# Kernel tuning notes

Hardware: AMD Instinct MI355X
Metric: run time of the kernel (lower is better)

Reference implementation:

```python
import jax, jax.numpy as jnp
import numpy as np

D_MODEL = 512
NUM_HEADS = 8
D_K = D_MODEL // NUM_HEADS


def setup_inputs() -> dict:
    key = jax.random.key(0)
    k0, k1, k2, k3, k4 = jax.random.split(key, 5)
    s = 1.0 / np.sqrt(D_MODEL)
    return {
        "x": jax.random.normal(k0, (2, 4096, D_MODEL), dtype=jnp.float32),
        "W_q": jax.random.normal(k1, (D_MODEL, D_MODEL), dtype=jnp.float32) * s,
        "W_k": jax.random.normal(k2, (D_MODEL, D_MODEL), dtype=jnp.float32) * s,
        "W_v": jax.random.normal(k3, (D_MODEL, D_MODEL), dtype=jnp.float32) * s,
        "W_o": jax.random.normal(k4, (D_MODEL, D_MODEL), dtype=jnp.float32) * s,
    }


def reference(x, W_q, W_k, W_v, W_o):
    B, S, _ = x.shape
    # project and split heads: (B, H, S, d_k)
    def split(t):
        return t.reshape(B, S, NUM_HEADS, D_K).transpose(0, 2, 1, 3)
    Q = split(x @ W_q)
    K = split(x @ W_k)
    V = split(x @ W_v)
    scale = jnp.sqrt(jnp.asarray(D_K, dtype=x.dtype))
    logits = jnp.einsum('bhqd,bhkd->bhqk', Q, K) / scale
    attn = jax.nn.softmax(logits, axis=-1)  # dropout is identity at inference
    out = jnp.einsum('bhqk,bhkd->bhqd', attn, V)
    concat = out.transpose(0, 2, 1, 3).reshape(B, S, D_MODEL)
    return concat @ W_o
```

## Files before the change

kernel.cpp:

```cpp
#include <hip/hip_runtime.h>
#include <hip/hip_bf16.h>


#define DMODEL 512
#define SEQ    4096
#define NTOK   8192
#define LDQK   1024

using f32x4 = __attribute__((ext_vector_type(4))) float;
using s16x8 = __attribute__((ext_vector_type(8))) short;
using u16x8 = __attribute__((ext_vector_type(8))) unsigned short;

static __device__ __forceinline__ unsigned short f2bf(float f) {
  union { float f; unsigned u; } v; v.f = f;
  unsigned r = v.u + 0x7fff + ((v.u >> 16) & 1);
  return (unsigned short)(r >> 16);
}

static __device__ __forceinline__ unsigned pack_bf2(float lo, float hi) {
  __hip_bfloat162 t = __float22bfloat162_rn(make_float2(lo, hi));
  union { __hip_bfloat162 b; unsigned u; } c; c.b = t; return c.u;
}

static __device__ __forceinline__ void gll16(const void* g, void* l) {
  __builtin_amdgcn_global_load_lds(
      (const __attribute__((address_space(1))) unsigned int*)g,
      (__attribute__((address_space(3))) unsigned int*)l, 16, 0, 0);
}

__global__ void prep_kernel(const float* __restrict__ x,
                            const float* __restrict__ Wq,
                            const float* __restrict__ Wk,
                            const float* __restrict__ Wv,
                            const float* __restrict__ Wo,
                            unsigned short* __restrict__ xb,
                            unsigned short* __restrict__ Wall, float c2) {
  __shared__ float T[64][65];
  const int bx = blockIdx.x;
  if (bx < 1024) {
    for (int i = bx * 256 + threadIdx.x; i < NTOK * DMODEL / 4; i += 262144) {
      float4 v = ((const float4*)x)[i];
      ushort4 o;
      o.x = f2bf(v.x); o.y = f2bf(v.y); o.z = f2bf(v.z); o.w = f2bf(v.w);
      ((ushort4*)xb)[i] = o;
    }
    return;
  }
  const int t = bx - 1024;
  const int y = t >> 6, sub = t & 63;
  const float* W = (y == 0) ? Wq : (y == 1) ? Wk : (y == 2) ? Wv : Wo;
  const float scale = (y == 0) ? c2 : 1.0f;
  const int tk = (sub & 7) * 64;
  const int tn = (sub >> 3) * 64;
  const int r  = threadIdx.x >> 2;
  const int cq = threadIdx.x & 3;
#pragma unroll
  for (int i = 0; i < 4; ++i) {
    int c = (cq + 4 * i) * 4;
    float4 v = *(const float4*)&W[(size_t)(tk + r) * 512 + tn + c];
    T[r][c + 0] = v.x * scale; T[r][c + 1] = v.y * scale;
    T[r][c + 2] = v.z * scale; T[r][c + 3] = v.w * scale;
  }
  __syncthreads();
  const int n  = threadIdx.x >> 2;
  const int k0 = (threadIdx.x & 3) * 16;
#pragma unroll
  for (int j4 = 0; j4 < 4; ++j4) {
    ushort4 o;
    o.x = f2bf(T[k0 + j4 * 4 + 0][n]);
    o.y = f2bf(T[k0 + j4 * 4 + 1][n]);
    o.z = f2bf(T[k0 + j4 * 4 + 2][n]);
    o.w = f2bf(T[k0 + j4 * 4 + 3][n]);
    *(ushort4*)&Wall[(size_t)y * 262144 + (size_t)(tn + n) * 512 + tk + k0 + j4 * 4] = o;
  }
}

__global__ __launch_bounds__(256, 3) void gemm_qkv(
    const unsigned short* __restrict__ xb,
    const unsigned short* __restrict__ Wall,
    unsigned short* __restrict__ QKb,
    unsigned short* __restrict__ Vtb)
{
  __shared__ unsigned short As[128 * 32];
  __shared__ unsigned short Bs[128 * 32];
  const int by = blockIdx.y;
  const bool vmode = (by >= 8);
  const unsigned short* A  = vmode ? (Wall + 2 * 262144) : xb;
  const unsigned short* Bt = vmode ? xb : Wall;
  const size_t bm = vmode ? (size_t)(by - 8) * 128 : (size_t)blockIdx.x * 128;
  const size_t bn = vmode ? (size_t)blockIdx.x * 128 : (size_t)by * 128;
  const int tid  = threadIdx.x;
  const int wave = tid >> 6, lane = tid & 63;
  const int q4 = lane >> 4, ln = lane & 15;
  const int wm = (wave >> 1) * 64, wn = (wave & 1) * 64;
  f32x4 acc[4][4] = {};
  const int srow = wave * 16 + (lane >> 2);
  const int scol = (lane & 3) * 8;

  const unsigned short* Ag  = A  + (bm + srow)      * 512 + scol;
  const unsigned short* Ag2 = A  + (bm + 64 + srow) * 512 + scol;
  const unsigned short* Bg  = Bt + (bn + srow)      * 512 + scol;
  const unsigned short* Bg2 = Bt + (bn + 64 + srow) * 512 + scol;
  unsigned short* Ad  = As + wave * 512;
  unsigned short* Ad2 = As + 2048 + wave * 512;
  unsigned short* Bd  = Bs + wave * 512;
  unsigned short* Bd2 = Bs + 2048 + wave * 512;

  for (int kt = 0; kt < 512; kt += 32) {
    __syncthreads();
    gll16(Ag + kt,  Ad);
    gll16(Ag2 + kt, Ad2);
    gll16(Bg + kt,  Bd);
    gll16(Bg2 + kt, Bd2);
    __syncthreads();
    s16x8 af[4], bfr[4];
#pragma unroll
    for (int i = 0; i < 4; i++)
      af[i] = *(const s16x8*)(As + (wm + i * 16 + ln) * 32 + q4 * 8);
#pragma unroll
    for (int i = 0; i < 4; i++)
      bfr[i] = *(const s16x8*)(Bs + (wn + i * 16 + ln) * 32 + q4 * 8);
#pragma unroll
    for (int mi = 0; mi < 4; mi++)
#pragma unroll
      for (int ni = 0; ni < 4; ni++)
        acc[mi][ni] = __builtin_amdgcn_mfma_f32_16x16x32_bf16(
            af[mi], bfr[ni], acc[mi][ni], 0, 0, 0);
  }
#pragma unroll
  for (int mi = 0; mi < 4; mi++)
#pragma unroll
    for (int r = 0; r < 4; ++r) {
      size_t row = bm + wm + mi * 16 + q4 * 4 + r;
#pragma unroll
      for (int ni = 0; ni < 4; ni++) {
        size_t col = bn + wn + ni * 16 + ln;
        unsigned short hv = f2bf(acc[mi][ni][r]);
        if (!vmode) {
          QKb[row * 1024 + col] = hv;
        } else {
          int b = (int)(col >> 12), s = (int)(col & 4095);
          int sp = (s & ~63) | (s & 32) | (((s >> 2) & 3) << 3) |
                   (((s >> 4) & 1) << 2) | (s & 3);
          Vtb[(size_t)b * 2097152 + row * 4096 + sp] = hv;
        }
      }
    }
}

__global__ __launch_bounds__(256, 2) void attn_kernel(
    const unsigned short* __restrict__ QK,
    const unsigned short* __restrict__ Vt,
    float* __restrict__ Opart,
    float* __restrict__ Lpart)
{
  const int qt = blockIdx.x, h = blockIdx.y, z = blockIdx.z;
  const int b = z >> 1, ck = z & 1;
  const int tid = threadIdx.x, wave = tid >> 6, lane = tid & 63;
  const int q4 = lane >> 4, ln = lane & 15;
  __shared__ unsigned short Ks[2][64 * 64];
  __shared__ unsigned short Vs[2][64 * 64];
  const size_t rowbase = (size_t)b * SEQ;
  const size_t qrow0   = (size_t)qt * 128 + wave * 32;
  const unsigned short* Kp  = QK + rowbase * LDQK + 512 + h * 64;
  const unsigned short* VTp = Vt + ((size_t)(b * 8 + h) * 64) * SEQ;

  s16x8 qf[2][2];
#pragma unroll
  for (int mf = 0; mf < 2; ++mf) {
    const unsigned short* q = QK + (rowbase + qrow0 + mf * 16 + ln) * LDQK + h * 64;
    qf[mf][0] = *(const s16x8*)(q + q4 * 8);
    qf[mf][1] = *(const s16x8*)(q + 32 + q4 * 8);
  }
  f32x4 o[2][4] = {};
  float lp[2] = {};

  const int srow = tid >> 2;
  const int c32  = (tid & 3) * 32;
  const int swz  = (srow & 7) << 4;
  const int wof0 = srow * 128 + ((c32 +  0) ^ swz);
  const int wof1 = srow * 128 + ((c32 + 16) ^ swz);
  const int rswz = (ln & 7) << 4;

  const unsigned short* kgp = Kp  + (size_t)(ck * 2048 + srow) * LDQK + (c32 >> 1);
  const unsigned short* vgp = VTp + (size_t)srow * SEQ + ck * 2048 + (c32 >> 1);

  u16x8 kr  = *(const u16x8*)kgp;
  u16x8 kr2 = *(const u16x8*)(kgp + 8);
  u16x8 vr  = *(const u16x8*)vgp;
  u16x8 vr2 = *(const u16x8*)(vgp + 8);
  *(u16x8*)((char*)Ks[0] + wof0) = kr;
  *(u16x8*)((char*)Ks[0] + wof1) = kr2;
  *(u16x8*)((char*)Vs[0] + wof0) = vr;
  *(u16x8*)((char*)Vs[0] + wof1) = vr2;
  kgp += (size_t)64 * LDQK;  vgp += 64;
  kr  = *(const u16x8*)kgp;
  kr2 = *(const u16x8*)(kgp + 8);
  vr  = *(const u16x8*)vgp;
  vr2 = *(const u16x8*)(vgp + 8);
  __syncthreads();

  const f32x4 fz = {0.f, 0.f, 0.f, 0.f};

  for (int t = 0; t < 32; ++t) {
    const int cur = t & 1;
    const char* Kc = (const char*)Ks[cur];
    const char* Vc = (const char*)Vs[cur];

    f32x4 s4[2][4];
#pragma unroll
    for (int ni = 0; ni < 4; ni++) {
      const char* kb = Kc + (ni * 16 + ln) * 128;
      s16x8 kf0 = *(const s16x8*)(kb + ((q4 * 16)      ^ rswz));
      s16x8 kf1 = *(const s16x8*)(kb + ((q4 * 16 + 64) ^ rswz));
      __builtin_amdgcn_s_setprio(1);
#pragma unroll
      for (int mf = 0; mf < 2; ++mf) {
        f32x4 acc0 = __builtin_amdgcn_mfma_f32_16x16x32_bf16(kf0, qf[mf][0], fz, 0, 0, 0);
        s4[mf][ni] = __builtin_amdgcn_mfma_f32_16x16x32_bf16(kf1, qf[mf][1], acc0, 0, 0, 0);
      }
      __builtin_amdgcn_s_setprio(0);
    }
    s16x8 vf[2][4];
#pragma unroll
    for (int ks = 0; ks < 2; ++ks)
#pragma unroll
      for (int ni = 0; ni < 4; ni++)
        vf[ks][ni] = *(const s16x8*)(Vc + (ni * 16 + ln) * 128 +
                                     ((ks * 64 + q4 * 16) ^ rswz));

    s16x8 pf[2][2];
#pragma unroll
    for (int mf = 0; mf < 2; ++mf) {
      float e[4][4];
#pragma unroll
      for (int ni = 0; ni < 4; ni++)
#pragma unroll
        for (int r = 0; r < 4; ++r)
          e[ni][r] = __builtin_amdgcn_exp2f(s4[mf][ni][r]);
      float t0 = (e[0][0] + e[0][1]) + (e[0][2] + e[0][3]);
      float t1 = (e[1][0] + e[1][1]) + (e[1][2] + e[1][3]);
      float t2 = (e[2][0] + e[2][1]) + (e[2][2] + e[2][3]);
      float t3 = (e[3][0] + e[3][1]) + (e[3][2] + e[3][3]);
      lp[mf] += (t0 + t1) + (t2 + t3);
#pragma unroll
      for (int ks = 0; ks < 2; ++ks) {
        union { s16x8 v; unsigned u[4]; } pu;
        pu.u[0] = pack_bf2(e[2 * ks][0],     e[2 * ks][1]);
        pu.u[1] = pack_bf2(e[2 * ks][2],     e[2 * ks][3]);
        pu.u[2] = pack_bf2(e[2 * ks + 1][0], e[2 * ks + 1][1]);
        pu.u[3] = pack_bf2(e[2 * ks + 1][2], e[2 * ks + 1][3]);
        pf[mf][ks] = pu.v;
      }
    }
    __builtin_amdgcn_s_setprio(1);
#pragma unroll
    for (int ks = 0; ks < 2; ++ks)
#pragma unroll
      for (int ni = 0; ni < 4; ni++)
#pragma unroll
        for (int mf = 0; mf < 2; ++mf)
          o[mf][ni] = __builtin_amdgcn_mfma_f32_16x16x32_bf16(pf[mf][ks], vf[ks][ni], o[mf][ni], 0, 0, 0);
    __builtin_amdgcn_s_setprio(0);

    if (t + 1 < 32) {
      char* Kn = (char*)Ks[cur ^ 1];
      char* Vn = (char*)Vs[cur ^ 1];
      *(u16x8*)(Kn + wof0) = kr;
      *(u16x8*)(Kn + wof1) = kr2;
      *(u16x8*)(Vn + wof0) = vr;
      *(u16x8*)(Vn + wof1) = vr2;
      if (t + 2 < 32) {
        kgp += (size_t)64 * LDQK;  vgp += 64;
        kr  = *(const u16x8*)kgp;
        kr2 = *(const u16x8*)(kgp + 8);
        vr  = *(const u16x8*)vgp;
        vr2 = *(const u16x8*)(vgp + 8);
      }
    }
    __syncthreads();
  }
#pragma unroll
  for (int mf = 0; mf < 2; ++mf) {
    float l = lp[mf];
    l += __shfl_xor(l, 16, 64);
    l += __shfl_xor(l, 32, 64);
    if (q4 == 0)
      Lpart[(size_t)ck * 65536 + (size_t)(b * 8 + h) * 4096 + qrow0 + mf * 16 + ln] = l;
  }
  float* Opc = Opart + (size_t)ck * NTOK * DMODEL;
#pragma unroll
  for (int mf = 0; mf < 2; ++mf)
#pragma unroll
    for (int r = 0; r < 4; ++r) {
      size_t row = rowbase + qrow0 + mf * 16 + q4 * 4 + r;
#pragma unroll
      for (int ni = 0; ni < 4; ni++)
        Opc[row * DMODEL + h * 64 + ni * 16 + ln] = o[mf][ni][r];
    }
}

__global__ void combine_kernel(const float* __restrict__ Opart,
                               const float* __restrict__ Lpart,
                               unsigned short* __restrict__ Oc) {
  int i = blockIdx.x * 256 + threadIdx.x;
  int row = i >> 7;
  int c4  = (i & 127) * 4;
  int b = row >> 12, qrow = row & 4095, h = c4 >> 6;
  float l = Lpart[(size_t)(b * 8 + h) * 4096 + qrow] +
            Lpart[65536 + (size_t)(b * 8 + h) * 4096 + qrow];
  float inv = 1.0f / l;
  f32x4 a = *(const f32x4*)(Opart + (size_t)row * 512 + c4);
  f32x4 c = *(const f32x4*)(Opart + (size_t)NTOK * DMODEL + (size_t)row * 512 + c4);
  float r0 = (a[0] + c[0]) * inv, r1 = (a[1] + c[1]) * inv;
  float r2 = (a[2] + c[2]) * inv, r3 = (a[3] + c[3]) * inv;
  uint2 w;
  w.x = pack_bf2(r0, r1);
  w.y = pack_bf2(r2, r3);
  *(uint2*)&Oc[(size_t)row * 512 + c4] = w;
}

__global__ __launch_bounds__(256, 3) void gemm_out(
    const unsigned short* __restrict__ A,
    const unsigned short* __restrict__ Bt,
    float* __restrict__ C)
{
  __shared__ unsigned short As[128 * 32];
  __shared__ unsigned short Bs[64 * 32];
  const int tid  = threadIdx.x;
  const int wave = tid >> 6, lane = tid & 63;
  const int q4 = lane >> 4, ln = lane & 15;
  const size_t bm = (size_t)blockIdx.x * 128;
  const size_t bn = (size_t)blockIdx.y * 64;
  const int wm = (wave >> 1) * 64, wn = (wave & 1) * 32;
  f32x4 acc[4][2] = {};
  const int srow = wave * 16 + (lane >> 2);
  const int scol = (lane & 3) * 8;

  const unsigned short* Ag  = A  + (bm + srow)      * 512 + scol;
  const unsigned short* Ag2 = A  + (bm + 64 + srow) * 512 + scol;
  const unsigned short* Bg  = Bt + (bn + srow)      * 512 + scol;
  unsigned short* Ad  = As + wave * 512;
  unsigned short* Ad2 = As + 2048 + wave * 512;
  unsigned short* Bd  = Bs + wave * 512;

  for (int kt = 0; kt < 512; kt += 32) {
    __syncthreads();
    gll16(Ag + kt,  Ad);
    gll16(Ag2 + kt, Ad2);
    gll16(Bg + kt,  Bd);
    __syncthreads();
    s16x8 af[4], bfr[2];
#pragma unroll
    for (int i = 0; i < 4; i++)
      af[i] = *(const s16x8*)(As + (wm + i * 16 + ln) * 32 + q4 * 8);
#pragma unroll
    for (int i = 0; i < 2; i++)
      bfr[i] = *(const s16x8*)(Bs + (wn + i * 16 + ln) * 32 + q4 * 8);
#pragma unroll
    for (int mi = 0; mi < 4; mi++)
#pragma unroll
      for (int ni = 0; ni < 2; ni++)
        acc[mi][ni] = __builtin_amdgcn_mfma_f32_16x16x32_bf16(
            af[mi], bfr[ni], acc[mi][ni], 0, 0, 0);
  }
#pragma unroll
  for (int mi = 0; mi < 4; mi++)
#pragma unroll
    for (int r = 0; r < 4; ++r) {
      size_t row = bm + wm + mi * 16 + q4 * 4 + r;
#pragma unroll
      for (int ni = 0; ni < 2; ni++)
        C[row * 512 + bn + wn + ni * 16 + ln] = acc[mi][ni][r];
    }
}

extern "C" void kernel_launch(void* const* d_in, const int* in_sizes, int n_in,
                              void* d_out, int out_size, void* d_ws, size_t ws_size,
                              hipStream_t stream) {
  const float* x  = (const float*)d_in[0];
  const float* Wq = (const float*)d_in[1];
  const float* Wk = (const float*)d_in[2];
  const float* Wv = (const float*)d_in[3];
  const float* Wo = (const float*)d_in[4];

  char* ws = (char*)d_ws;
  unsigned short* xb    = (unsigned short*)(ws);
  unsigned short* Wall  = (unsigned short*)(ws + 8388608);
  unsigned short* QKb   = (unsigned short*)(ws + 10485760);
  unsigned short* Vtb   = (unsigned short*)(ws + 27262976);
  unsigned short* Oc    = (unsigned short*)(ws + 35651584);
  float*          Opart = (float*)(ws + 44040192);
  float*          Lpart = (float*)(ws + 77594624);

  const float C2 = 0.125f * 1.44269504088896f;

  hipLaunchKernelGGL(prep_kernel, dim3(1280), dim3(256), 0, stream,
                     x, Wq, Wk, Wv, Wo, xb, Wall, C2);
  hipLaunchKernelGGL(gemm_qkv, dim3(64, 12), dim3(256), 0, stream,
                     xb, Wall, QKb, Vtb);
  hipLaunchKernelGGL(attn_kernel, dim3(32, 8, 4), dim3(256), 0, stream,
                     QKb, Vtb, Opart, Lpart);
  hipLaunchKernelGGL(combine_kernel, dim3(4096), dim3(256), 0, stream,
                     Opart, Lpart, Oc);
  hipLaunchKernelGGL(gemm_out, dim3(64, 8), dim3(256), 0, stream,
                     Oc, Wall + 3 * 262144, (float*)d_out);
}
```

Before: 193.2 us.

## Drop split-K attention and fuse normalization into attention epilogue

The attention kernel no longer splits the key range in two. Each block now handles 64 query rows (16 per wave) across all 4096 keys and writes normalized bf16 output directly, so the combine kernel and the fp32 partial O/L buffers are removed. The grid is remapped with a block-index swizzle so blocks sharing a head run close together, and launch bounds are raised to 4 blocks per CU. This removes a launch and the fp32 partial write/read traffic. In exchange, K/V tiles are reused across fewer query rows, so K/V loads per unit of work double, and each block runs twice as many loop iterations.

Result: slower. 203.3 us (+5.2%).

```diff
diff --git a/kernel.cpp b/kernel.cpp
--- a/kernel.cpp
+++ b/kernel.cpp
@@ -148,32 +148,31 @@
     }
 }
 
-__global__ __launch_bounds__(256, 2) void attn_kernel(
+__global__ __launch_bounds__(256, 4) void attn_kernel(
     const unsigned short* __restrict__ QK,
     const unsigned short* __restrict__ Vt,
-    float* __restrict__ Opart,
-    float* __restrict__ Lpart)
+    unsigned short* __restrict__ Oc)
 {
-  const int qt = blockIdx.x, h = blockIdx.y, z = blockIdx.z;
-  const int b = z >> 1, ck = z & 1;
+  const int bid = blockIdx.x + 64 * (blockIdx.y + 8 * blockIdx.z);
+  const int lin = (bid & 7) * 128 + (bid >> 3);
+  const int qt = lin & 63, h = (lin >> 6) & 7, b = lin >> 9;
   const int tid = threadIdx.x, wave = tid >> 6, lane = tid & 63;
   const int q4 = lane >> 4, ln = lane & 15;
   __shared__ unsigned short Ks[2][64 * 64];
   __shared__ unsigned short Vs[2][64 * 64];
   const size_t rowbase = (size_t)b * SEQ;
-  const size_t qrow0   = (size_t)qt * 128 + wave * 32;
+  const size_t qrow0   = (size_t)qt * 64 + wave * 16;
   const unsigned short* Kp  = QK + rowbase * LDQK + 512 + h * 64;
   const unsigned short* VTp = Vt + ((size_t)(b * 8 + h) * 64) * SEQ;
 
-  s16x8 qf[2][2];
-#pragma unroll
-  for (int mf = 0; mf < 2; ++mf) {
-    const unsigned short* q = QK + (rowbase + qrow0 + mf * 16 + ln) * LDQK + h * 64;
-    qf[mf][0] = *(const s16x8*)(q + q4 * 8);
-    qf[mf][1] = *(const s16x8*)(q + 32 + q4 * 8);
-  }
-  f32x4 o[2][4] = {};
-  float lp[2] = {};
+  s16x8 qf[2];
+  {
+    const unsigned short* q = QK + (rowbase + qrow0 + ln) * LDQK + h * 64;
+    qf[0] = *(const s16x8*)(q + q4 * 8);
+    qf[1] = *(const s16x8*)(q + 32 + q4 * 8);
+  }
+  f32x4 o[4] = {};
+  float lp = 0.f;
 
   const int srow = tid >> 2;
   const int c32  = (tid & 3) * 32;
@@ -182,8 +181,8 @@
   const int wof1 = srow * 128 + ((c32 + 16) ^ swz);
   const int rswz = (ln & 7) << 4;
 
-  const unsigned short* kgp = Kp  + (size_t)(ck * 2048 + srow) * LDQK + (c32 >> 1);
-  const unsigned short* vgp = VTp + (size_t)srow * SEQ + ck * 2048 + (c32 >> 1);
+  const unsigned short* kgp = Kp  + (size_t)srow * LDQK + (c32 >> 1);
+  const unsigned short* vgp = VTp + (size_t)srow * SEQ + (c32 >> 1);
 
   u16x8 kr  = *(const u16x8*)kgp;
   u16x8 kr2 = *(const u16x8*)(kgp + 8);
@@ -202,23 +201,20 @@
 
   const f32x4 fz = {0.f, 0.f, 0.f, 0.f};
 
-  for (int t = 0; t < 32; ++t) {
+  for (int t = 0; t < 64; ++t) {
     const int cur = t & 1;
     const char* Kc = (const char*)Ks[cur];
     const char* Vc = (const char*)Vs[cur];
 
-    f32x4 s4[2][4];
+    f32x4 s4[4];
 #pragma unroll
     for (int ni = 0; ni < 4; ni++) {
       const char* kb = Kc + (ni * 16 + ln) * 128;
       s16x8 kf0 = *(const s16x8*)(kb + ((q4 * 16)      ^ rswz));
       s16x8 kf1 = *(const s16x8*)(kb + ((q4 * 16 + 64) ^ rswz));
       __builtin_amdgcn_s_setprio(1);
-#pragma unroll
-      for (int mf = 0; mf < 2; ++mf) {
-        f32x4 acc0 = __builtin_amdgcn_mfma_f32_16x16x32_bf16(kf0, qf[mf][0], fz, 0, 0, 0);
-        s4[mf][ni] = __builtin_amdgcn_mfma_f32_16x16x32_bf16(kf1, qf[mf][1], acc0, 0, 0, 0);
-      }
+      f32x4 acc0 = __builtin_amdgcn_mfma_f32_16x16x32_bf16(kf0, qf[0], fz, 0, 0, 0);
+      s4[ni] = __builtin_amdgcn_mfma_f32_16x16x32_bf16(kf1, qf[1], acc0, 0, 0, 0);
       __builtin_amdgcn_s_setprio(0);
     }
     s16x8 vf[2][4];
@@ -229,20 +225,19 @@
         vf[ks][ni] = *(const s16x8*)(Vc + (ni * 16 + ln) * 128 +
                                      ((ks * 64 + q4 * 16) ^ rswz));
 
-    s16x8 pf[2][2];
-#pragma unroll
-    for (int mf = 0; mf < 2; ++mf) {
+    s16x8 pf[2];
+    {
       float e[4][4];
 #pragma unroll
       for (int ni = 0; ni < 4; ni++)
 #pragma unroll
         for (int r = 0; r < 4; ++r)
-          e[ni][r] = __builtin_amdgcn_exp2f(s4[mf][ni][r]);
+          e[ni][r] = __builtin_amdgcn_exp2f(s4[ni][r]);
       float t0 = (e[0][0] + e[0][1]) + (e[0][2] + e[0][3]);
       float t1 = (e[1][0] + e[1][1]) + (e[1][2] + e[1][3]);
       float t2 = (e[2][0] + e[2][1]) + (e[2][2] + e[2][3]);
       float t3 = (e[3][0] + e[3][1]) + (e[3][2] + e[3][3]);
-      lp[mf] += (t0 + t1) + (t2 + t3);
+      lp += (t0 + t1) + (t2 + t3);
 #pragma unroll
       for (int ks = 0; ks < 2; ++ks) {
         union { s16x8 v; unsigned u[4]; } pu;
@@ -250,7 +245,7 @@
         pu.u[1] = pack_bf2(e[2 * ks][2],     e[2 * ks][3]);
         pu.u[2] = pack_bf2(e[2 * ks + 1][0], e[2 * ks + 1][1]);
         pu.u[3] = pack_bf2(e[2 * ks + 1][2], e[2 * ks + 1][3]);
-        pf[mf][ks] = pu.v;
+        pf[ks] = pu.v;
       }
     }
     __builtin_amdgcn_s_setprio(1);
@@ -258,19 +253,17 @@
     for (int ks = 0; ks < 2; ++ks)
 #pragma unroll
       for (int ni = 0; ni < 4; ni++)
-#pragma unroll
-        for (int mf = 0; mf < 2; ++mf)
-          o[mf][ni] = __builtin_amdgcn_mfma_f32_16x16x32_bf16(pf[mf][ks], vf[ks][ni], o[mf][ni], 0, 0, 0);
+        o[ni] = __builtin_amdgcn_mfma_f32_16x16x32_bf16(pf[ks], vf[ks][ni], o[ni], 0, 0, 0);
     __builtin_amdgcn_s_setprio(0);
 
-    if (t + 1 < 32) {
+    if (t + 1 < 64) {
       char* Kn = (char*)Ks[cur ^ 1];
       char* Vn = (char*)Vs[cur ^ 1];
       *(u16x8*)(Kn + wof0) = kr;
       *(u16x8*)(Kn + wof1) = kr2;
       *(u16x8*)(Vn + wof0) = vr;
       *(u16x8*)(Vn + wof1) = vr2;
-      if (t + 2 < 32) {
+      if (t + 2 < 64) {
         kgp += (size_t)64 * LDQK;  vgp += 64;
         kr  = *(const u16x8*)kgp;
         kr2 = *(const u16x8*)(kgp + 8);
@@ -280,44 +273,18 @@
     }
     __syncthreads();
   }
-#pragma unroll
-  for (int mf = 0; mf < 2; ++mf) {
-    float l = lp[mf];
-    l += __shfl_xor(l, 16, 64);
-    l += __shfl_xor(l, 32, 64);
-    if (q4 == 0)
-      Lpart[(size_t)ck * 65536 + (size_t)(b * 8 + h) * 4096 + qrow0 + mf * 16 + ln] = l;
-  }
-  float* Opc = Opart + (size_t)ck * NTOK * DMODEL;
-#pragma unroll
-  for (int mf = 0; mf < 2; ++mf)
-#pragma unroll
-    for (int r = 0; r < 4; ++r) {
-      size_t row = rowbase + qrow0 + mf * 16 + q4 * 4 + r;
-#pragma unroll
-      for (int ni = 0; ni < 4; ni++)
-        Opc[row * DMODEL + h * 64 + ni * 16 + ln] = o[mf][ni][r];
-    }
-}
-
-__global__ void combine_kernel(const float* __restrict__ Opart,
-                               const float* __restrict__ Lpart,
-                               unsigned short* __restrict__ Oc) {
-  int i = blockIdx.x * 256 + threadIdx.x;
-  int row = i >> 7;
-  int c4  = (i & 127) * 4;
-  int b = row >> 12, qrow = row & 4095, h = c4 >> 6;
-  float l = Lpart[(size_t)(b * 8 + h) * 4096 + qrow] +
-            Lpart[65536 + (size_t)(b * 8 + h) * 4096 + qrow];
-  float inv = 1.0f / l;
-  f32x4 a = *(const f32x4*)(Opart + (size_t)row * 512 + c4);
-  f32x4 c = *(const f32x4*)(Opart + (size_t)NTOK * DMODEL + (size_t)row * 512 + c4);
-  float r0 = (a[0] + c[0]) * inv, r1 = (a[1] + c[1]) * inv;
-  float r2 = (a[2] + c[2]) * inv, r3 = (a[3] + c[3]) * inv;
-  uint2 w;
-  w.x = pack_bf2(r0, r1);
-  w.y = pack_bf2(r2, r3);
-  *(uint2*)&Oc[(size_t)row * 512 + c4] = w;
+  float l = lp;
+  l += __shfl_xor(l, 16, 64);
+  l += __shfl_xor(l, 32, 64);
+  const float inv = 1.0f / l;
+#pragma unroll
+  for (int r = 0; r < 4; ++r) {
+    const float nv = __shfl(inv, q4 * 4 + r, 64);
+    const size_t row = rowbase + qrow0 + q4 * 4 + r;
+#pragma unroll
+    for (int ni = 0; ni < 4; ni++)
+      Oc[row * 512 + h * 64 + ni * 16 + ln] = f2bf(o[ni][r] * nv);
+  }
 }
 
 __global__ __launch_bounds__(256, 3) void gemm_out(
@@ -390,8 +357,6 @@
   unsigned short* QKb   = (unsigned short*)(ws + 10485760);
   unsigned short* Vtb   = (unsigned short*)(ws + 27262976);
   unsigned short* Oc    = (unsigned short*)(ws + 35651584);
-  float*          Opart = (float*)(ws + 44040192);
-  float*          Lpart = (float*)(ws + 77594624);
 
   const float C2 = 0.125f * 1.44269504088896f;
 
@@ -399,10 +364,8 @@
                      x, Wq, Wk, Wv, Wo, xb, Wall, C2);
   hipLaunchKernelGGL(gemm_qkv, dim3(64, 12), dim3(256), 0, stream,
                      xb, Wall, QKb, Vtb);
-  hipLaunchKernelGGL(attn_kernel, dim3(32, 8, 4), dim3(256), 0, stream,
-                     QKb, Vtb, Opart, Lpart);
-  hipLaunchKernelGGL(combine_kernel, dim3(4096), dim3(256), 0, stream,
-                     Opart, Lpart, Oc);
+  hipLaunchKernelGGL(attn_kernel, dim3(64, 8, 2), dim3(256), 0, stream,
+                     QKb, Vtb, Oc);
   hipLaunchKernelGGL(gemm_out, dim3(64, 8), dim3(256), 0, stream,
                      Oc, Wall + 3 * 262144, (float*)d_out);
 }
```

## Drop split-KV attention and fuse normalization into attention epilogue

Applied to the files above, without the earlier changes.

The attention kernel now processes the full 4096-key sequence per block instead of splitting keys into two halves. It normalizes the output in-register and writes bf16 directly, which removes the fp32 partial output and row-sum buffers and the separate combine kernel. Blocks are also remapped so that consecutive block IDs are spread across heads and batches, which may improve L2 locality across XCDs. The trade-off is half as many blocks (512 instead of 1024) with twice the serial loop length, which lowers parallelism and occupancy slack on a large GPU.

After: 191.0 us. Within noise of the previous version (-1.1%).

```diff
diff --git a/kernel.cpp b/kernel.cpp
--- a/kernel.cpp
+++ b/kernel.cpp
@@ -151,11 +151,12 @@
 __global__ __launch_bounds__(256, 2) void attn_kernel(
     const unsigned short* __restrict__ QK,
     const unsigned short* __restrict__ Vt,
-    float* __restrict__ Opart,
-    float* __restrict__ Lpart)
+    unsigned short* __restrict__ Oc)
 {
-  const int qt = blockIdx.x, h = blockIdx.y, z = blockIdx.z;
-  const int b = z >> 1, ck = z & 1;
+  const int bid = blockIdx.x + 32 * (blockIdx.y + 8 * blockIdx.z);
+  const int lin = (bid & 7) * 64 + (bid >> 3);
+  const int qt = lin & 31, bh = lin >> 5;
+  const int h = bh & 7, b = bh >> 3;
   const int tid = threadIdx.x, wave = tid >> 6, lane = tid & 63;
   const int q4 = lane >> 4, ln = lane & 15;
   __shared__ unsigned short Ks[2][64 * 64];
@@ -182,8 +183,8 @@
   const int wof1 = srow * 128 + ((c32 + 16) ^ swz);
   const int rswz = (ln & 7) << 4;
 
-  const unsigned short* kgp = Kp  + (size_t)(ck * 2048 + srow) * LDQK + (c32 >> 1);
-  const unsigned short* vgp = VTp + (size_t)srow * SEQ + ck * 2048 + (c32 >> 1);
+  const unsigned short* kgp = Kp  + (size_t)srow * LDQK + (c32 >> 1);
+  const unsigned short* vgp = VTp + (size_t)srow * SEQ + (c32 >> 1);
 
   u16x8 kr  = *(const u16x8*)kgp;
   u16x8 kr2 = *(const u16x8*)(kgp + 8);
@@ -202,7 +203,7 @@
 
   const f32x4 fz = {0.f, 0.f, 0.f, 0.f};
 
-  for (int t = 0; t < 32; ++t) {
+  for (int t = 0; t < 64; ++t) {
     const int cur = t & 1;
     const char* Kc = (const char*)Ks[cur];
     const char* Vc = (const char*)Vs[cur];
@@ -263,14 +264,14 @@
           o[mf][ni] = __builtin_amdgcn_mfma_f32_16x16x32_bf16(pf[mf][ks], vf[ks][ni], o[mf][ni], 0, 0, 0);
     __builtin_amdgcn_s_setprio(0);
 
-    if (t + 1 < 32) {
+    if (t + 1 < 64) {
       char* Kn = (char*)Ks[cur ^ 1];
       char* Vn = (char*)Vs[cur ^ 1];
       *(u16x8*)(Kn + wof0) = kr;
       *(u16x8*)(Kn + wof1) = kr2;
       *(u16x8*)(Vn + wof0) = vr;
       *(u16x8*)(Vn + wof1) = vr2;
-      if (t + 2 < 32) {
+      if (t + 2 < 64) {
         kgp += (size_t)64 * LDQK;  vgp += 64;
         kr  = *(const u16x8*)kgp;
         kr2 = *(const u16x8*)(kgp + 8);
@@ -285,39 +286,16 @@
     float l = lp[mf];
     l += __shfl_xor(l, 16, 64);
     l += __shfl_xor(l, 32, 64);
-    if (q4 == 0)
-      Lpart[(size_t)ck * 65536 + (size_t)(b * 8 + h) * 4096 + qrow0 + mf * 16 + ln] = l;
-  }
-  float* Opc = Opart + (size_t)ck * NTOK * DMODEL;
-#pragma unroll
-  for (int mf = 0; mf < 2; ++mf)
+    const float inv = 1.0f / l;
 #pragma unroll
     for (int r = 0; r < 4; ++r) {
-      size_t row = rowbase + qrow0 + mf * 16 + q4 * 4 + r;
-#pragma unroll
-      for (int ni = 0; ni < 4; ni++)
-        Opc[row * DMODEL + h * 64 + ni * 16 + ln] = o[mf][ni][r];
-    }
-}
-
-__global__ void combine_kernel(const float* __restrict__ Opart,
-                               const float* __restrict__ Lpart,
-                               unsigned short* __restrict__ Oc) {
-  int i = blockIdx.x * 256 + threadIdx.x;
-  int row = i >> 7;
-  int c4  = (i & 127) * 4;
-  int b = row >> 12, qrow = row & 4095, h = c4 >> 6;
-  float l = Lpart[(size_t)(b * 8 + h) * 4096 + qrow] +
-            Lpart[65536 + (size_t)(b * 8 + h) * 4096 + qrow];
-  float inv = 1.0f / l;
-  f32x4 a = *(const f32x4*)(Opart + (size_t)row * 512 + c4);
-  f32x4 c = *(const f32x4*)(Opart + (size_t)NTOK * DMODEL + (size_t)row * 512 + c4);
-  float r0 = (a[0] + c[0]) * inv, r1 = (a[1] + c[1]) * inv;
-  float r2 = (a[2] + c[2]) * inv, r3 = (a[3] + c[3]) * inv;
-  uint2 w;
-  w.x = pack_bf2(r0, r1);
-  w.y = pack_bf2(r2, r3);
-  *(uint2*)&Oc[(size_t)row * 512 + c4] = w;
+      const float nv = __shfl(inv, q4 * 4 + r, 64);
+      const size_t row = rowbase + qrow0 + mf * 16 + q4 * 4 + r;
+#pragma unroll
+      for (int ni = 0; ni < 4; ni++)
+        Oc[row * 512 + h * 64 + ni * 16 + ln] = f2bf(o[mf][ni][r] * nv);
+    }
+  }
 }
 
 __global__ __launch_bounds__(256, 3) void gemm_out(
@@ -390,8 +368,6 @@
   unsigned short* QKb   = (unsigned short*)(ws + 10485760);
   unsigned short* Vtb   = (unsigned short*)(ws + 27262976);
   unsigned short* Oc    = (unsigned short*)(ws + 35651584);
-  float*          Opart = (float*)(ws + 44040192);
-  float*          Lpart = (float*)(ws + 77594624);
 
   const float C2 = 0.125f * 1.44269504088896f;
 
@@ -399,10 +375,8 @@
                      x, Wq, Wk, Wv, Wo, xb, Wall, C2);
   hipLaunchKernelGGL(gemm_qkv, dim3(64, 12), dim3(256), 0, stream,
                      xb, Wall, QKb, Vtb);
-  hipLaunchKernelGGL(attn_kernel, dim3(32, 8, 4), dim3(256), 0, stream,
-                     QKb, Vtb, Opart, Lpart);
-  hipLaunchKernelGGL(combine_kernel, dim3(4096), dim3(256), 0, stream,
-                     Opart, Lpart, Oc);
+  hipLaunchKernelGGL(attn_kernel, dim3(32, 8, 2), dim3(256), 0, stream,
+                     QKb, Vtb, Oc);
   hipLaunchKernelGGL(gemm_out, dim3(64, 8), dim3(256), 0, stream,
                      Oc, Wall + 3 * 262144, (float*)d_out);
 }
```
